# Performance work log

Hardware: AMD Instinct MI355X
Metric: run time of the kernel (lower is better)

The kernel has to match this reference:

```python
import jax, jax.numpy as jnp
import numpy as np

D_MODEL = 1024
NUM_HEADS = 16
D_K = D_MODEL // NUM_HEADS


def setup_inputs() -> dict:
    key = jax.random.key(0)
    ks = jax.random.split(key, 9)
    s = 1.0 / np.sqrt(D_MODEL)
    x = jax.random.normal(ks[0], (2, 2048, D_MODEL), dtype=jnp.float32)
    Wq = jax.random.uniform(ks[1], (D_MODEL, D_MODEL), jnp.float32, -s, s)
    bq = jax.random.uniform(ks[2], (D_MODEL,), jnp.float32, -s, s)
    Wk = jax.random.uniform(ks[3], (D_MODEL, D_MODEL), jnp.float32, -s, s)
    bk = jax.random.uniform(ks[4], (D_MODEL,), jnp.float32, -s, s)
    Wv = jax.random.uniform(ks[5], (D_MODEL, D_MODEL), jnp.float32, -s, s)
    bv = jax.random.uniform(ks[6], (D_MODEL,), jnp.float32, -s, s)
    Wo = jax.random.uniform(ks[7], (D_MODEL, D_MODEL), jnp.float32, -s, s)
    bo = jax.random.uniform(ks[8], (D_MODEL,), jnp.float32, -s, s)
    return {"x": x, "Wq": Wq, "bq": bq, "Wk": Wk, "bk": bk,
            "Wv": Wv, "bv": bv, "Wo": Wo, "bo": bo}


def reference(x, Wq, bq, Wk, bk, Wv, bv, Wo, bo):
    B, S, _ = x.shape
    # projections (torch Linear: x @ W.T + b; here W stored as [in, out])
    q = (x @ Wq + bq).reshape(B, S, NUM_HEADS, D_K).transpose(0, 2, 1, 3)
    k = (x @ Wk + bk).reshape(B, S, NUM_HEADS, D_K).transpose(0, 2, 1, 3)
    v = (x @ Wv + bv).reshape(B, S, NUM_HEADS, D_K).transpose(0, 2, 1, 3)
    scores = jnp.einsum('bhqd,bhkd->bhqk', q, k) / jnp.sqrt(jnp.float32(D_K))
    attn = jax.nn.softmax(scores, axis=-1)
    out = jnp.einsum('bhqk,bhkd->bhqd', attn, v)  # [B,H,S,Dk]
    out = out.transpose(0, 2, 1, 3).reshape(B, S, D_MODEL)
    return out @ Wo + bo
```

## Files before the change

kernel.cpp:

```cpp
#include <hip/hip_runtime.h>

#define SEQ   2048
#define DM    1024
#define NH    16
#define DK    64
#define BATCH 2
#define M_TOT 4096
#define C1 0.18033688011112042f

typedef __attribute__((ext_vector_type(8))) short bf16x8;
typedef __attribute__((ext_vector_type(4))) float f32x4;
typedef unsigned short u16;

__device__ inline u16 f2b(float f) {
    union { float f; unsigned u; } x; x.f = f;
    return (u16)((x.u + 0x7FFFu + ((x.u >> 16) & 1u)) >> 16);
}

__device__ inline void async_cp16(const u16* g, u16* l) {
    __builtin_amdgcn_global_load_lds(
        (const __attribute__((address_space(1))) unsigned int*)g,
        (__attribute__((address_space(3))) unsigned int*)l, 16, 0, 0);
}

__global__ __launch_bounds__(256) void cast_x(
    const float4* __restrict__ x, ushort4* __restrict__ xb)
{
    int gid = blockIdx.x * 256 + threadIdx.x;
    float4 v = x[gid];
    ushort4 o;
    o.x = f2b(v.x); o.y = f2b(v.y); o.z = f2b(v.z); o.w = f2b(v.w);
    xb[gid] = o;
}

__global__ __launch_bounds__(256) void transpose_cast4(
    const float* __restrict__ W0, const float* __restrict__ W1,
    const float* __restrict__ W2, const float* __restrict__ W3,
    u16* __restrict__ WtBase)
{
    __shared__ float tile[32][33];
    const int t = threadIdx.x;
    const int n0 = blockIdx.x << 5, k0 = blockIdx.y << 5, z = blockIdx.z;
    const float* W = (z == 0) ? W0 : (z == 1) ? W1 : (z == 2) ? W2 : W3;
    u16* Wt = WtBase + (size_t)z * DM * DM;
    #pragma unroll
    for (int i = 0; i < 4; ++i) {
        int idx = t + (i << 8); int r = idx >> 5, c = idx & 31;
        tile[r][c] = W[(size_t)(k0 + r) * DM + n0 + c];
    }
    __syncthreads();
    #pragma unroll
    for (int i = 0; i < 4; ++i) {
        int idx = t + (i << 8); int r = idx >> 5, c = idx & 31;
        Wt[(size_t)(n0 + r) * DM + k0 + c] = f2b(tile[c][r]);
    }
}

__global__ __launch_bounds__(256) void gemm_bt(
    const u16* __restrict__ A, const u16* __restrict__ Bt, int mode,
    const float* __restrict__ bias0, const float* __restrict__ bias1,
    const float* __restrict__ bias2,
    void* __restrict__ out0, void* __restrict__ out1, void* __restrict__ out2)
{
    __shared__ u16 sh[128 * 32 * 2];
    u16* As = sh;
    u16* Bs = sh + 128 * 32;
    const int t = threadIdx.x, wid = t >> 6, lane = t & 63;
    const int lr = lane & 15, quad = lane >> 4;
    const int m0 = blockIdx.y << 7, n0 = blockIdx.x << 7;
    const int wm = (wid & 1) << 6, wn = (wid >> 1) << 6;
    const int rowA = lane >> 2;
    const int colA = (((lane & 3) - ((lane >> 3) & 3)) & 3) << 3;
    const int sA = (((lr >> 1) + quad) & 3) << 3;

    f32x4 acc[4][4];
    #pragma unroll
    for (int i = 0; i < 4; ++i)
        #pragma unroll
        for (int j = 0; j < 4; ++j) acc[i][j] = (f32x4){0.f, 0.f, 0.f, 0.f};

    for (int k0 = 0; k0 < DM; k0 += 32) {
        #pragma unroll
        for (int i = 0; i < 2; ++i) {
            int ch = wid * 2 + i;
            async_cp16(A  + (size_t)(m0 + ch * 16 + rowA) * DM + k0 + colA,
                       As + ch * 16 * 32);
            async_cp16(Bt + (size_t)(n0 + ch * 16 + rowA) * DM + k0 + colA,
                       Bs + ch * 16 * 32);
        }
        __syncthreads();
        bf16x8 af[4], bfr[4];
        #pragma unroll
        for (int mt = 0; mt < 4; ++mt)
            af[mt] = *(const bf16x8*)(As + (wm + 16 * mt + lr) * 32 + sA);
        #pragma unroll
        for (int nt = 0; nt < 4; ++nt)
            bfr[nt] = *(const bf16x8*)(Bs + (wn + 16 * nt + lr) * 32 + sA);
        #pragma unroll
        for (int mt = 0; mt < 4; ++mt)
            #pragma unroll
            for (int nt = 0; nt < 4; ++nt)
                acc[mt][nt] = __builtin_amdgcn_mfma_f32_16x16x32_bf16(
                    af[mt], bfr[nt], acc[mt][nt], 0, 0, 0);
        __syncthreads();
    }

    if (mode == 1) {
        u16* wstrip = sh + wid * 1152;
        const int ngb = n0 + wn;
        const int which = ngb >> 10, nnb = ngb & 1023;
        const int h = nnb >> 6;
        const float* bp = (which == 0) ? bias0 : (which == 1) ? bias1 : bias2;
        const float sc = (which == 0) ? C1 : 1.0f;
        float bias_v[4];
        #pragma unroll
        for (int nt = 0; nt < 4; ++nt) bias_v[nt] = bp[nnb + 16 * nt + lr];

        if (which < 2) {
            u16* dst = which ? (u16*)out1 : (u16*)out0;
            #pragma unroll
            for (int mt = 0; mt < 4; ++mt) {
                #pragma unroll
                for (int nt = 0; nt < 4; ++nt)
                    #pragma unroll
                    for (int r = 0; r < 4; ++r)
                        wstrip[(quad * 4 + r) * 72 + 16 * nt + lr] =
                            f2b((acc[mt][nt][r] + bias_v[nt]) * sc);
                asm volatile("s_waitcnt lgkmcnt(0)" ::: "memory");
                #pragma unroll
                for (int half = 0; half < 2; ++half) {
                    int id = lane + 64 * half;
                    int mloc = id >> 3, dl = (id & 7) << 3;
                    int m = m0 + wm + 16 * mt + mloc;
                    int b = m >> 11, s = m & (SEQ - 1);
                    *(uint4*)(dst + ((size_t)(b * NH + h) * SEQ + s) * DK + dl) =
                        *(const uint4*)(wstrip + mloc * 72 + dl);
                }
                asm volatile("s_waitcnt lgkmcnt(0)" ::: "memory");
            }
        } else {
            u16* dst = (u16*)out2;
            #pragma unroll
            for (int mt = 0; mt < 4; ++mt) {
                #pragma unroll
                for (int nt = 0; nt < 4; ++nt)
                    #pragma unroll
                    for (int r = 0; r < 4; ++r)
                        wstrip[(16 * nt + lr) * 16 + quad * 4 + r] =
                            f2b(acc[mt][nt][r] + bias_v[nt]);
                asm volatile("s_waitcnt lgkmcnt(0)" ::: "memory");
                #pragma unroll
                for (int half = 0; half < 2; ++half) {
                    int id = lane + 64 * half;
                    int d = id >> 1, cho = (id & 1) << 3;
                    int m = m0 + wm + 16 * mt + cho;
                    int b = m >> 11, s = m & (SEQ - 1);
                    *(uint4*)(dst + ((size_t)(b * NH + h) * DK + d) * SEQ + s) =
                        *(const uint4*)(wstrip + d * 16 + cho);
                }
                asm volatile("s_waitcnt lgkmcnt(0)" ::: "memory");
            }
        }
    } else {
        float* O = (float*)out0;
        #pragma unroll
        for (int nt = 0; nt < 4; ++nt) {
            int ng = n0 + wn + 16 * nt + lr;
            float bv_ = bias0[ng];
            #pragma unroll
            for (int mt = 0; mt < 4; ++mt) {
                int mr = m0 + wm + 16 * mt + (quad << 2);
                f32x4 v = acc[mt][nt];
                O[(size_t)mr * DM + ng]       = v.x + bv_;
                O[(size_t)(mr + 1) * DM + ng] = v.y + bv_;
                O[(size_t)(mr + 2) * DM + ng] = v.z + bv_;
                O[(size_t)(mr + 3) * DM + ng] = v.w + bv_;
            }
        }
    }
}

__global__ __launch_bounds__(256) void attn_mfma(
    const u16* __restrict__ Q, const u16* __restrict__ K,
    const u16* __restrict__ Vt, u16* __restrict__ A)
{
    __shared__ u16 sh[20480];

    const int t = threadIdx.x, wid = t >> 6, lane = t & 63;
    const int lr = lane & 15, quad = lane >> 4;
    const int bx = blockIdx.x;
    const int xcd = bx & 7, within = bx >> 3;
    const int bh  = xcd * 4 + (within >> 5);
    const int q0  = (within & 31) << 6;

    const u16* Kb = K  + (size_t)bh * SEQ * DK;
    const u16* Vb = Vt + (size_t)bh * DK * SEQ;

    const u16* qp = Q + ((size_t)bh * SEQ + q0 + 16 * wid + lr) * DK + quad * 8;
    bf16x8 bQ0 = *(const bf16x8*)(qp);
    bf16x8 bQ1 = *(const bf16x8*)(qp + 32);

    f32x4 O[4];
    #pragma unroll
    for (int mt = 0; mt < 4; ++mt) O[mt] = (f32x4){0.f, 0.f, 0.f, 0.f};
    float l_r = 0.f;

    const int srow = t >> 3, schunk = t & 7;
    const int sslot = ((schunk ^ (srow & 7)) << 3);
    const int soff0 = srow * 64 + sslot;
    const int soff1 = (srow + 32) * 64 + sslot;
    const int c0 = ((quad ^ (lr & 7)) << 3);
    const int c1 = (((quad + 4) ^ (lr & 7)) << 3);
    const int prow = 16384 + (16 * wid + lr) * 64;

    uint4 kr0 = *(const uint4*)(Kb + (size_t)srow * DK + schunk * 8);
    uint4 kr1 = *(const uint4*)(Kb + (size_t)(srow + 32) * DK + schunk * 8);
    uint4 vr0 = *(const uint4*)(Vb + (size_t)srow * SEQ + schunk * 8);
    uint4 vr1 = *(const uint4*)(Vb + (size_t)(srow + 32) * SEQ + schunk * 8);
    *(uint4*)(sh + soff0) = kr0;
    *(uint4*)(sh + soff1) = kr1;
    *(uint4*)(sh + 8192 + soff0) = vr0;
    *(uint4*)(sh + 8192 + soff1) = vr1;
    kr0 = *(const uint4*)(Kb + (size_t)(64 + srow) * DK + schunk * 8);
    kr1 = *(const uint4*)(Kb + (size_t)(64 + srow + 32) * DK + schunk * 8);
    vr0 = *(const uint4*)(Vb + (size_t)srow * SEQ + 64 + schunk * 8);
    vr1 = *(const uint4*)(Vb + (size_t)(srow + 32) * SEQ + 64 + schunk * 8);
    __syncthreads();

    for (int it = 0; it < SEQ / 64; ++it) {
        const int kbase = (it & 1) << 12;
        const int vbase = 8192 + ((it & 1) << 12);

        f32x4 S[4];
        #pragma unroll
        for (int mt = 0; mt < 4; ++mt) {
            bf16x8 a0 = *(const bf16x8*)(sh + kbase + (16 * mt + lr) * 64 + c0);
            bf16x8 a1 = *(const bf16x8*)(sh + kbase + (16 * mt + lr) * 64 + c1);
            f32x4 s = (f32x4){0.f, 0.f, 0.f, 0.f};
            s = __builtin_amdgcn_mfma_f32_16x16x32_bf16(a0, bQ0, s, 0, 0, 0);
            s = __builtin_amdgcn_mfma_f32_16x16x32_bf16(a1, bQ1, s, 0, 0, 0);
            S[mt] = s;
        }

        #pragma unroll
        for (int mt = 0; mt < 4; ++mt) {
            float e0 = __builtin_amdgcn_exp2f(S[mt][0]);
            float e1 = __builtin_amdgcn_exp2f(S[mt][1]);
            float e2 = __builtin_amdgcn_exp2f(S[mt][2]);
            float e3 = __builtin_amdgcn_exp2f(S[mt][3]);
            l_r += (e0 + e1) + (e2 + e3);
            ushort4 pk;
            pk.x = f2b(e0); pk.y = f2b(e1); pk.z = f2b(e2); pk.w = f2b(e3);
            int chunk = 2 * mt + (quad >> 1);
            *(ushort4*)(sh + prow + ((chunk ^ (lr & 7)) << 3)
                           + ((quad & 1) << 2)) = pk;
        }
        asm volatile("s_waitcnt lgkmcnt(0)" ::: "memory");

        bf16x8 p0 = *(const bf16x8*)(sh + prow + c0);
        bf16x8 p1 = *(const bf16x8*)(sh + prow + c1);
        #pragma unroll
        for (int mt = 0; mt < 4; ++mt) {
            bf16x8 v0 = *(const bf16x8*)(sh + vbase + (16 * mt + lr) * 64 + c0);
            bf16x8 v1 = *(const bf16x8*)(sh + vbase + (16 * mt + lr) * 64 + c1);
            O[mt] = __builtin_amdgcn_mfma_f32_16x16x32_bf16(v0, p0, O[mt], 0, 0, 0);
            O[mt] = __builtin_amdgcn_mfma_f32_16x16x32_bf16(v1, p1, O[mt], 0, 0, 0);
        }

        if (it < SEQ / 64 - 1) {
            const int kn = ((it + 1) & 1) << 12;
            const int vn = 8192 + (((it + 1) & 1) << 12);
            *(uint4*)(sh + kn + soff0) = kr0;
            *(uint4*)(sh + kn + soff1) = kr1;
            *(uint4*)(sh + vn + soff0) = vr0;
            *(uint4*)(sh + vn + soff1) = vr1;
            if (it < SEQ / 64 - 2) {
                int nt2 = (it + 2) * 64;
                kr0 = *(const uint4*)(Kb + (size_t)(nt2 + srow) * DK + schunk * 8);
                kr1 = *(const uint4*)(Kb + (size_t)(nt2 + srow + 32) * DK + schunk * 8);
                vr0 = *(const uint4*)(Vb + (size_t)srow * SEQ + nt2 + schunk * 8);
                vr1 = *(const uint4*)(Vb + (size_t)(srow + 32) * SEQ + nt2 + schunk * 8);
            }
            __syncthreads();
        }
    }

    l_r += __shfl_xor(l_r, 16);
    l_r += __shfl_xor(l_r, 32);

    const int b = bh >> 4, h = bh & 15;
    const int q = q0 + 16 * wid + lr;
    float inv = 1.f / l_r;
    #pragma unroll
    for (int mt = 0; mt < 4; ++mt) {
        ushort4 pk;
        pk.x = f2b(O[mt][0] * inv); pk.y = f2b(O[mt][1] * inv);
        pk.z = f2b(O[mt][2] * inv); pk.w = f2b(O[mt][3] * inv);
        *(ushort4*)(A + (size_t)(b * SEQ + q) * DM + h * DK + 16 * mt + 4 * quad) = pk;
    }
}

extern "C" void kernel_launch(void* const* d_in, const int* in_sizes, int n_in,
                              void* d_out, int out_size, void* d_ws, size_t ws_size,
                              hipStream_t stream)
{
    const float* x  = (const float*)d_in[0];
    const float* Wq = (const float*)d_in[1];
    const float* bq = (const float*)d_in[2];
    const float* Wk = (const float*)d_in[3];
    const float* bk = (const float*)d_in[4];
    const float* Wv = (const float*)d_in[5];
    const float* bv = (const float*)d_in[6];
    const float* Wo = (const float*)d_in[7];
    const float* bo = (const float*)d_in[8];

    const size_t NE = (size_t)M_TOT * DM;
    u16* xb     = (u16*)d_ws;
    u16* wt_qkv = xb + NE;
    u16* wt_o   = wt_qkv + 3 * (size_t)DM * DM;
    u16* q_ws   = wt_o + (size_t)DM * DM;
    u16* k_ws   = q_ws + NE;
    u16* vt_ws  = k_ws + NE;
    u16* a_ws   = vt_ws + NE;

    cast_x<<<M_TOT * DM / 4 / 256, 256, 0, stream>>>((const float4*)x, (ushort4*)xb);
    transpose_cast4<<<dim3(32, 32, 4), 256, 0, stream>>>(Wq, Wk, Wv, Wo, wt_qkv);

    gemm_bt<<<dim3(24, 32), 256, 0, stream>>>(
        xb, wt_qkv, 1, bq, bk, bv, q_ws, k_ws, vt_ws);

    attn_mfma<<<dim3(1024), 256, 0, stream>>>(q_ws, k_ws, vt_ws, a_ws);

    gemm_bt<<<dim3(8, 32), 256, 0, stream>>>(
        a_ws, wt_o, 0, bo, nullptr, nullptr, d_out, nullptr, nullptr);
}
```

Baseline: 217.9 us.

## Double GEMM K-tile to 64, transpose Q layout, use packed bf16 conversions

The GEMM main loop now loads 64-wide K tiles with an XOR-swizzled LDS layout, which halves the number of barrier pairs per tile. Q is written transposed, like V, by the projection epilogue, and attention gathers Q with strided scalar loads. Float-to-bf16 conversions use the packed two-element intrinsic throughout. The changes trade a larger LDS footprint and an uncoalesced Q load for fewer synchronisations and cheaper conversions.

```diff
diff --git a/kernel.cpp b/kernel.cpp
--- a/kernel.cpp
+++ b/kernel.cpp
@@ -1,4 +1,5 @@
 #include <hip/hip_runtime.h>
+#include <hip/hip_bf16.h>
 
 #define SEQ   2048
 #define DM    1024
@@ -17,6 +18,11 @@
     return (u16)((x.u + 0x7FFFu + ((x.u >> 16) & 1u)) >> 16);
 }
 
+__device__ inline unsigned pk2(float a, float b) {
+    __hip_bfloat162 h = __float22bfloat162_rn(make_float2(a, b));
+    return *reinterpret_cast<unsigned*>(&h);
+}
+
 __device__ inline void async_cp16(const u16* g, u16* l) {
     __builtin_amdgcn_global_load_lds(
         (const __attribute__((address_space(1))) unsigned int*)g,
@@ -24,12 +30,12 @@
 }
 
 __global__ __launch_bounds__(256) void cast_x(
-    const float4* __restrict__ x, ushort4* __restrict__ xb)
+    const float4* __restrict__ x, uint2* __restrict__ xb)
 {
     int gid = blockIdx.x * 256 + threadIdx.x;
     float4 v = x[gid];
-    ushort4 o;
-    o.x = f2b(v.x); o.y = f2b(v.y); o.z = f2b(v.z); o.w = f2b(v.w);
+    uint2 o;
+    o.x = pk2(v.x, v.y); o.y = pk2(v.z, v.w);
     xb[gid] = o;
 }
 
@@ -62,16 +68,17 @@
     const float* __restrict__ bias2,
     void* __restrict__ out0, void* __restrict__ out1, void* __restrict__ out2)
 {
-    __shared__ u16 sh[128 * 32 * 2];
+    __shared__ u16 sh[128 * 64 * 2];
     u16* As = sh;
-    u16* Bs = sh + 128 * 32;
+    u16* Bs = sh + 128 * 64;
     const int t = threadIdx.x, wid = t >> 6, lane = t & 63;
     const int lr = lane & 15, quad = lane >> 4;
     const int m0 = blockIdx.y << 7, n0 = blockIdx.x << 7;
     const int wm = (wid & 1) << 6, wn = (wid >> 1) << 6;
-    const int rowA = lane >> 2;
-    const int colA = (((lane & 3) - ((lane >> 3) & 3)) & 3) << 3;
-    const int sA = (((lr >> 1) + quad) & 3) << 3;
+    const int lrow = lane >> 3;
+    const int scol = (((lane & 7) ^ lrow) << 3);
+    const int c0 = ((quad ^ (lr & 7)) << 3);
+    const int c1 = (((quad + 4) ^ (lr & 7)) << 3);
 
     f32x4 acc[4][4];
     #pragma unroll
@@ -79,29 +86,31 @@
         #pragma unroll
         for (int j = 0; j < 4; ++j) acc[i][j] = (f32x4){0.f, 0.f, 0.f, 0.f};
 
-    for (int k0 = 0; k0 < DM; k0 += 32) {
-        #pragma unroll
-        for (int i = 0; i < 2; ++i) {
-            int ch = wid * 2 + i;
-            async_cp16(A  + (size_t)(m0 + ch * 16 + rowA) * DM + k0 + colA,
-                       As + ch * 16 * 32);
-            async_cp16(Bt + (size_t)(n0 + ch * 16 + rowA) * DM + k0 + colA,
-                       Bs + ch * 16 * 32);
+    for (int k0 = 0; k0 < DM; k0 += 64) {
+        #pragma unroll
+        for (int i = 0; i < 4; ++i) {
+            int rb = 32 * i + 8 * wid;
+            async_cp16(A  + (size_t)(m0 + rb + lrow) * DM + k0 + scol, As + rb * 64);
+            async_cp16(Bt + (size_t)(n0 + rb + lrow) * DM + k0 + scol, Bs + rb * 64);
         }
         __syncthreads();
-        bf16x8 af[4], bfr[4];
-        #pragma unroll
-        for (int mt = 0; mt < 4; ++mt)
-            af[mt] = *(const bf16x8*)(As + (wm + 16 * mt + lr) * 32 + sA);
-        #pragma unroll
-        for (int nt = 0; nt < 4; ++nt)
-            bfr[nt] = *(const bf16x8*)(Bs + (wn + 16 * nt + lr) * 32 + sA);
-        #pragma unroll
-        for (int mt = 0; mt < 4; ++mt)
+        #pragma unroll
+        for (int h = 0; h < 2; ++h) {
+            const int cc = h ? c1 : c0;
+            bf16x8 af[4], bfr[4];
+            #pragma unroll
+            for (int mt = 0; mt < 4; ++mt)
+                af[mt] = *(const bf16x8*)(As + (wm + 16 * mt + lr) * 64 + cc);
             #pragma unroll
             for (int nt = 0; nt < 4; ++nt)
-                acc[mt][nt] = __builtin_amdgcn_mfma_f32_16x16x32_bf16(
-                    af[mt], bfr[nt], acc[mt][nt], 0, 0, 0);
+                bfr[nt] = *(const bf16x8*)(Bs + (wn + 16 * nt + lr) * 64 + cc);
+            #pragma unroll
+            for (int mt = 0; mt < 4; ++mt)
+                #pragma unroll
+                for (int nt = 0; nt < 4; ++nt)
+                    acc[mt][nt] = __builtin_amdgcn_mfma_f32_16x16x32_bf16(
+                        af[mt], bfr[nt], acc[mt][nt], 0, 0, 0);
+        }
         __syncthreads();
     }
 
@@ -116,8 +125,33 @@
         #pragma unroll
         for (int nt = 0; nt < 4; ++nt) bias_v[nt] = bp[nnb + 16 * nt + lr];
 
-        if (which < 2) {
-            u16* dst = which ? (u16*)out1 : (u16*)out0;
+        if (which != 1) {
+            u16* dst = (which == 0) ? (u16*)out0 : (u16*)out2;
+            #pragma unroll
+            for (int mt = 0; mt < 4; ++mt) {
+                #pragma unroll
+                for (int nt = 0; nt < 4; ++nt) {
+                    uint2 w;
+                    w.x = pk2((acc[mt][nt][0] + bias_v[nt]) * sc,
+                              (acc[mt][nt][1] + bias_v[nt]) * sc);
+                    w.y = pk2((acc[mt][nt][2] + bias_v[nt]) * sc,
+                              (acc[mt][nt][3] + bias_v[nt]) * sc);
+                    *(uint2*)(wstrip + (16 * nt + lr) * 16 + quad * 4) = w;
+                }
+                asm volatile("s_waitcnt lgkmcnt(0)" ::: "memory");
+                #pragma unroll
+                for (int half = 0; half < 2; ++half) {
+                    int id = lane + 64 * half;
+                    int d = id >> 1, cho = (id & 1) << 3;
+                    int m = m0 + wm + 16 * mt + cho;
+                    int b = m >> 11, s = m & (SEQ - 1);
+                    *(uint4*)(dst + ((size_t)(b * NH + h) * DK + d) * SEQ + s) =
+                        *(const uint4*)(wstrip + d * 16 + cho);
+                }
+                asm volatile("s_waitcnt lgkmcnt(0)" ::: "memory");
+            }
+        } else {
+            u16* dst = (u16*)out1;
             #pragma unroll
             for (int mt = 0; mt < 4; ++mt) {
                 #pragma unroll
@@ -125,7 +159,7 @@
                     #pragma unroll
                     for (int r = 0; r < 4; ++r)
                         wstrip[(quad * 4 + r) * 72 + 16 * nt + lr] =
-                            f2b((acc[mt][nt][r] + bias_v[nt]) * sc);
+                            f2b(acc[mt][nt][r] + bias_v[nt]);
                 asm volatile("s_waitcnt lgkmcnt(0)" ::: "memory");
                 #pragma unroll
                 for (int half = 0; half < 2; ++half) {
@@ -138,28 +172,6 @@
                 }
                 asm volatile("s_waitcnt lgkmcnt(0)" ::: "memory");
             }
-        } else {
-            u16* dst = (u16*)out2;
-            #pragma unroll
-            for (int mt = 0; mt < 4; ++mt) {
-                #pragma unroll
-                for (int nt = 0; nt < 4; ++nt)
-                    #pragma unroll
-                    for (int r = 0; r < 4; ++r)
-                        wstrip[(16 * nt + lr) * 16 + quad * 4 + r] =
-                            f2b(acc[mt][nt][r] + bias_v[nt]);
-                asm volatile("s_waitcnt lgkmcnt(0)" ::: "memory");
-                #pragma unroll
-                for (int half = 0; half < 2; ++half) {
-                    int id = lane + 64 * half;
-                    int d = id >> 1, cho = (id & 1) << 3;
-                    int m = m0 + wm + 16 * mt + cho;
-                    int b = m >> 11, s = m & (SEQ - 1);
-                    *(uint4*)(dst + ((size_t)(b * NH + h) * DK + d) * SEQ + s) =
-                        *(const uint4*)(wstrip + d * 16 + cho);
-                }
-                asm volatile("s_waitcnt lgkmcnt(0)" ::: "memory");
-            }
         }
     } else {
         float* O = (float*)out0;
@@ -181,7 +193,7 @@
 }
 
 __global__ __launch_bounds__(256) void attn_mfma(
-    const u16* __restrict__ Q, const u16* __restrict__ K,
+    const u16* __restrict__ Qt, const u16* __restrict__ K,
     const u16* __restrict__ Vt, u16* __restrict__ A)
 {
     __shared__ u16 sh[20480];
@@ -196,9 +208,14 @@
     const u16* Kb = K  + (size_t)bh * SEQ * DK;
     const u16* Vb = Vt + (size_t)bh * DK * SEQ;
 
-    const u16* qp = Q + ((size_t)bh * SEQ + q0 + 16 * wid + lr) * DK + quad * 8;
-    bf16x8 bQ0 = *(const bf16x8*)(qp);
-    bf16x8 bQ1 = *(const bf16x8*)(qp + 32);
+    const int q = q0 + 16 * wid + lr;
+    const u16* Qb = Qt + (size_t)bh * DK * SEQ + q;
+    bf16x8 bQ0, bQ1;
+    #pragma unroll
+    for (int j = 0; j < 8; ++j) {
+        bQ0[j] = (short)Qb[(size_t)(quad * 8 + j) * SEQ];
+        bQ1[j] = (short)Qb[(size_t)(32 + quad * 8 + j) * SEQ];
+    }
 
     f32x4 O[4];
     #pragma unroll
@@ -249,11 +266,11 @@
             float e2 = __builtin_amdgcn_exp2f(S[mt][2]);
             float e3 = __builtin_amdgcn_exp2f(S[mt][3]);
             l_r += (e0 + e1) + (e2 + e3);
-            ushort4 pk;
-            pk.x = f2b(e0); pk.y = f2b(e1); pk.z = f2b(e2); pk.w = f2b(e3);
+            uint2 pk;
+            pk.x = pk2(e0, e1); pk.y = pk2(e2, e3);
             int chunk = 2 * mt + (quad >> 1);
-            *(ushort4*)(sh + prow + ((chunk ^ (lr & 7)) << 3)
-                           + ((quad & 1) << 2)) = pk;
+            *(uint2*)(sh + prow + ((chunk ^ (lr & 7)) << 3)
+                         + ((quad & 1) << 2)) = pk;
         }
         asm volatile("s_waitcnt lgkmcnt(0)" ::: "memory");
 
@@ -289,14 +306,13 @@
     l_r += __shfl_xor(l_r, 32);
 
     const int b = bh >> 4, h = bh & 15;
-    const int q = q0 + 16 * wid + lr;
     float inv = 1.f / l_r;
     #pragma unroll
     for (int mt = 0; mt < 4; ++mt) {
-        ushort4 pk;
-        pk.x = f2b(O[mt][0] * inv); pk.y = f2b(O[mt][1] * inv);
-        pk.z = f2b(O[mt][2] * inv); pk.w = f2b(O[mt][3] * inv);
-        *(ushort4*)(A + (size_t)(b * SEQ + q) * DM + h * DK + 16 * mt + 4 * quad) = pk;
+        uint2 pk;
+        pk.x = pk2(O[mt][0] * inv, O[mt][1] * inv);
+        pk.y = pk2(O[mt][2] * inv, O[mt][3] * inv);
+        *(uint2*)(A + (size_t)(b * SEQ + q) * DM + h * DK + 16 * mt + 4 * quad) = pk;
     }
 }
 
@@ -318,18 +334,18 @@
     u16* xb     = (u16*)d_ws;
     u16* wt_qkv = xb + NE;
     u16* wt_o   = wt_qkv + 3 * (size_t)DM * DM;
-    u16* q_ws   = wt_o + (size_t)DM * DM;
-    u16* k_ws   = q_ws + NE;
+    u16* qt_ws  = wt_o + (size_t)DM * DM;
+    u16* k_ws   = qt_ws + NE;
     u16* vt_ws  = k_ws + NE;
     u16* a_ws   = vt_ws + NE;
 
-    cast_x<<<M_TOT * DM / 4 / 256, 256, 0, stream>>>((const float4*)x, (ushort4*)xb);
+    cast_x<<<M_TOT * DM / 4 / 256, 256, 0, stream>>>((const float4*)x, (uint2*)xb);
     transpose_cast4<<<dim3(32, 32, 4), 256, 0, stream>>>(Wq, Wk, Wv, Wo, wt_qkv);
 
     gemm_bt<<<dim3(24, 32), 256, 0, stream>>>(
-        xb, wt_qkv, 1, bq, bk, bv, q_ws, k_ws, vt_ws);
-
-    attn_mfma<<<dim3(1024), 256, 0, stream>>>(q_ws, k_ws, vt_ws, a_ws);
+        xb, wt_qkv, 1, bq, bk, bv, qt_ws, k_ws, vt_ws);
+
+    attn_mfma<<<dim3(1024), 256, 0, stream>>>(qt_ws, k_ws, vt_ws, a_ws);
 
     gemm_bt<<<dim3(8, 32), 256, 0, stream>>>(
         a_ws, wt_o, 0, bo, nullptr, nullptr, d_out, nullptr, nullptr);
```

Result: slower. 228.4 us (+4.8%).
